# Performance work log

Hardware: AMD Instinct MI355X
Metric: run time of the kernel (lower is better)

## Reference

```python
import jax, jax.numpy as jnp
import numpy as np

B, L = 256, 100
N100, N10_100, N0_10 = 40000, 80000, 120000
D100, D10_100, D0_10 = 500, 250, 250  # layers[0]/2, layers[0]/4, remainder
H1, H2 = 200, 1000                    # layers = [1000, 200, 1000]
NUM_PIX = N100 + N10_100 + N0_10


def setup_inputs() -> dict:
    key = jax.random.key(0)
    ks = jax.random.split(key, 11)
    rn = lambda k, shape, scale: jax.random.normal(k, shape, jnp.float32) * scale
    return {
        'songs_bucket': jax.random.randint(ks[0], (B, L), 0, 3, jnp.int32),
        'songs_id': jax.random.randint(ks[1], (B, L), 0, N100, jnp.int32),
        'W100': rn(ks[2], (N100, D100), 0.02),
        'W10_100': rn(ks[3], (N10_100, D10_100), 0.02),
        'W0_10': rn(ks[4], (N0_10, D0_10), 0.02),
        'fc1_w': rn(ks[5], (H1, 1000), 0.03),
        'fc1_b': jnp.zeros((H1,), jnp.float32),
        'fc2_w': rn(ks[6], (H2, H1), 0.07),
        'fc2_b': jnp.zeros((H2,), jnp.float32),
        'out_w': rn(ks[7], (NUM_PIX, H2), 0.03),
        'out_b': jnp.zeros((NUM_PIX,), jnp.float32),
    }


def _masked_mean(table, ids, mask):
    # table: [V, D], ids: [B, L], mask: [B, L] bool -> [B, D]
    emb = table[ids]                                   # gather [B, L, D]
    m = mask.astype(emb.dtype)
    ssum = jnp.einsum('bl,bld->bd', m, emb)            # masked segment-sum
    cnt = m.sum(axis=1)                                # [B]
    mean = ssum / jnp.maximum(cnt, 1.0)[:, None]
    return jnp.where(cnt[:, None] > 0, mean, 0.0)     # empty bucket -> zeros


def reference(songs_bucket, songs_id, W100, W10_100, W0_10,
              fc1_w, fc1_b, fc2_w, fc2_b, out_w, out_b):
    # per-bucket masked embedding mean (vectorized embedding-bag)
    e0 = _masked_mean(W100, songs_id, songs_bucket == 0)       # [B, 500]
    e1 = _masked_mean(W10_100, songs_id, songs_bucket == 1)    # [B, 250]
    e2 = _masked_mean(W0_10, songs_id, songs_bucket == 2)      # [B, 250]
    x = jnp.concatenate([e0, e1, e2], axis=-1)                 # [B, 1000]
    # tiny MLP (dropout p=False -> p=0, a no-op)
    h = jax.nn.relu(x @ fc1_w.T + fc1_b)                       # [B, 200]
    h = jax.nn.relu(h @ fc2_w.T + fc2_b)                       # [B, 1000]
    ratings = h @ out_w.T + out_b                              # [B, NUM_PIX]
    return ratings
```

## Files before the change

kernel.cpp:

```cpp
#include <hip/hip_runtime.h>

#define NUM_B 256
#define SEQ_L 100
#define NPIX  240000
#define KPAD  1024
#define BN    128
#define BK    128
#define NWG   1875

typedef __attribute__((ext_vector_type(8))) short short8;
typedef __attribute__((ext_vector_type(4))) float f32x4;

static __device__ __forceinline__ unsigned short f2bf(float f) {
  unsigned int u = __builtin_bit_cast(unsigned int, f);
  u += 0x7fffu + ((u >> 16) & 1u);
  return (unsigned short)(u >> 16);
}

__global__ __launch_bounds__(1024) void embed_mlp_kernel(
    const int* __restrict__ bucket, const int* __restrict__ ids,
    const float* __restrict__ W100, const float* __restrict__ W10,
    const float* __restrict__ W0,
    const float* __restrict__ fc1_w, const float* __restrict__ fc1_b,
    const float* __restrict__ fc2_w, const float* __restrict__ fc2_b,
    unsigned short* __restrict__ h2out)
{
  __shared__ __align__(16) float xw[16][1000];
  __shared__ __align__(16) float xs[1000];
  __shared__ __align__(16) float h1s[200];
  __shared__ int sb[SEQ_L], sid[SEQ_L];
  __shared__ int cnt[16][3];
  __shared__ int cntT[3];

  const int row = blockIdx.x, tid = threadIdx.x;
  const int wid = tid >> 6, lane = tid & 63;

  if (tid < SEQ_L) {
    sb[tid]  = bucket[row * SEQ_L + tid];
    sid[tid] = ids[row * SEQ_L + tid];
  }
  __syncthreads();

  float acc0[8] = {0,0,0,0,0,0,0,0};
  float acc1[4] = {0,0,0,0};
  float acc2[4] = {0,0,0,0};
  int c0 = 0, c1 = 0, c2 = 0;

  for (int l = wid; l < SEQ_L; l += 16) {
    const int b = sb[l];
    const long id = sid[l];
    if (b == 0) {
      ++c0; const float* r = W100 + id * 500;
      #pragma unroll
      for (int j = 0; j < 7; ++j) acc0[j] += r[lane + 64 * j];
      if (lane < 52) acc0[7] += r[lane + 448];
    } else if (b == 1) {
      ++c1; const float* r = W10 + id * 250;
      #pragma unroll
      for (int j = 0; j < 3; ++j) acc1[j] += r[lane + 64 * j];
      if (lane < 58) acc1[3] += r[lane + 192];
    } else {
      ++c2; const float* r = W0 + id * 250;
      #pragma unroll
      for (int j = 0; j < 3; ++j) acc2[j] += r[lane + 64 * j];
      if (lane < 58) acc2[3] += r[lane + 192];
    }
  }
  {
    float* xp = xw[wid];
    #pragma unroll
    for (int j = 0; j < 8; ++j) { int d = lane + 64 * j; if (d < 500) xp[d] = acc0[j]; }
    #pragma unroll
    for (int j = 0; j < 4; ++j) { int d = lane + 64 * j; if (d < 250) xp[500 + d] = acc1[j]; }
    #pragma unroll
    for (int j = 0; j < 4; ++j) { int d = lane + 64 * j; if (d < 250) xp[750 + d] = acc2[j]; }
    if (lane == 0) { cnt[wid][0] = c0; cnt[wid][1] = c1; cnt[wid][2] = c2; }
  }
  __syncthreads();
  if (tid < 3) { int s = 0; for (int w = 0; w < 16; ++w) s += cnt[w][tid]; cntT[tid] = s; }
  __syncthreads();
  if (tid < 1000) {
    float s = 0.f;
    #pragma unroll
    for (int w = 0; w < 16; ++w) s += xw[w][tid];
    const int bkt = tid < 500 ? 0 : (tid < 750 ? 1 : 2);
    const int c = cntT[bkt];
    xs[tid] = c ? s / (float)c : 0.f;
  }
  __syncthreads();

  const int g = tid >> 4, sl = tid & 15;

  for (int o = g; o < 200; o += 64) {
    const f32x4* wr = (const f32x4*)(fc1_w + o * 1000);
    const f32x4* xv = (const f32x4*)xs;
    float p = 0.f;
    for (int j = sl; j < 250; j += 16) {
      f32x4 a = xv[j], b = wr[j];
      p += a.x * b.x + a.y * b.y + a.z * b.z + a.w * b.w;
    }
    #pragma unroll
    for (int off = 8; off; off >>= 1) p += __shfl_down(p, off, 16);
    if (sl == 0) h1s[o] = fmaxf(p + fc1_b[o], 0.f);
  }
  __syncthreads();

  unsigned short* hrow = h2out + (long)row * KPAD;
  for (int o = g; o < 1000; o += 64) {
    const f32x4* wr = (const f32x4*)(fc2_w + o * 200);
    const f32x4* hv = (const f32x4*)h1s;
    float p = 0.f;
    #pragma unroll
    for (int j = sl; j < 50; j += 16) {
      f32x4 a = hv[j], b = wr[j];
      p += a.x * b.x + a.y * b.y + a.z * b.z + a.w * b.w;
    }
    #pragma unroll
    for (int off = 8; off; off >>= 1) p += __shfl_down(p, off, 16);
    if (sl == 0) hrow[o] = f2bf(fmaxf(p + fc2_b[o], 0.f));
  }
  if (tid < KPAD - 1000) hrow[1000 + tid] = 0;
}

__global__ __launch_bounds__(512) void out_gemm_kernel(
    const unsigned short* __restrict__ h2,
    const float* __restrict__ out_w,
    const float* __restrict__ out_b,
    float* __restrict__ out)
{
  __shared__ __align__(16) unsigned char lds[98304];
  unsigned char* As = lds;
  unsigned char* Bs = lds + 65536;

  const int tid = threadIdx.x;

  const int q = NWG / 8, r = NWG % 8;
  const int xcd = blockIdx.x & 7, bidx = blockIdx.x >> 3;
  const int wg = (xcd < r ? xcd * (q + 1) : r * (q + 1) + (xcd - r) * q) + bidx;
  const long n0 = (long)wg * BN;

  const f32x4 fz = {0.f, 0.f, 0.f, 0.f};

  f32x4 bReg[8];

  auto dmaA = [&](int kt) {
    #pragma unroll
    for (int i = 0; i < 8; ++i) {
      const int c = tid + 512 * i;
      const int rw = c >> 4;
      const int k16s = (c & 15) ^ (rw & 7);
      const unsigned short* src = h2 + rw * KPAD + kt * BK + k16s * 8;
      __builtin_amdgcn_global_load_lds(
          (const __attribute__((address_space(1))) void*)src,
          (__attribute__((address_space(3))) void*)(As + c * 16),
          16, 0, 0);
    }
  };
  auto loadB = [&](int k0) {
    #pragma unroll
    for (int i = 0; i < 8; ++i) {
      int c = tid + 512 * i;
      int n = c >> 5, qq = c & 31;
      int k = k0 + qq * 4;
      bReg[i] = (k < 1000)
        ? __builtin_nontemporal_load((const f32x4*)(out_w + (long)(n0 + n) * 1000 + k))
        : fz;
    }
  };
  auto storeB = [&]() {
    #pragma unroll
    for (int i = 0; i < 8; ++i) {
      int c = tid + 512 * i;
      int n = c >> 5, qq = c & 31;
      ushort4 h;
      h.x = f2bf(bReg[i].x); h.y = f2bf(bReg[i].y);
      h.z = f2bf(bReg[i].z); h.w = f2bf(bReg[i].w);
      *(ushort4*)(Bs + n * 256 + ((qq * 8) ^ ((n & 7) << 4))) = h;
    }
  };

  const int wid = tid >> 6, lane = tid & 63;
  const int wm = wid >> 2, wn = wid & 3;
  const int lrow = lane & 15, lkg = lane >> 4;

  f32x4 acc[8][2];
  #pragma unroll
  for (int m = 0; m < 8; ++m) { acc[m][0] = fz; acc[m][1] = fz; }

  dmaA(0); loadB(0);
  #pragma unroll 1
  for (int kt = 0; kt < 8; ++kt) {
    storeB();
    __syncthreads();
    if (kt < 7) loadB((kt + 1) * BK);
    #pragma unroll
    for (int kk = 0; kk < 4; ++kk) {
      short8 bf[2];
      #pragma unroll
      for (int n = 0; n < 2; ++n) {
        int nr = wn * 32 + n * 16 + lrow;
        bf[n] = *(const short8*)(Bs + nr * 256 + (((kk * 64) + lkg * 16) ^ ((nr & 7) << 4)));
      }
      #pragma unroll
      for (int m = 0; m < 8; ++m) {
        int rr = wm * 128 + m * 16 + lrow;
        short8 af = *(const short8*)(As + rr * 256 + (((kk * 64) + lkg * 16) ^ ((rr & 7) << 4)));
        acc[m][0] = __builtin_amdgcn_mfma_f32_16x16x32_bf16(af, bf[0], acc[m][0], 0, 0, 0);
        acc[m][1] = __builtin_amdgcn_mfma_f32_16x16x32_bf16(af, bf[1], acc[m][1], 0, 0, 0);
      }
    }
    __syncthreads();
    if (kt < 7) dmaA((kt + 1) * 0 + kt + 1);
  }

  const float b0 = out_b[n0 + wn * 32 + lrow];
  const float b1 = out_b[n0 + wn * 32 + 16 + lrow];
  float* E = (float*)lds;
  #pragma unroll
  for (int half = 0; half < 2; ++half) {
    __syncthreads();
    if (wm == half) {
      #pragma unroll
      for (int m = 0; m < 8; ++m) {
        #pragma unroll
        for (int n = 0; n < 2; ++n) {
          const int col = wn * 32 + n * 16 + lrow;
          const float bias = n ? b1 : b0;
          #pragma unroll
          for (int rr = 0; rr < 4; ++rr) {
            const int rowl = m * 16 + lkg * 4 + rr;
            E[rowl * 132 + col] = acc[m][n][rr] + bias;
          }
        }
      }
    }
    __syncthreads();
    const int rbase = half * 128;
    #pragma unroll
    for (int s = 0; s < 8; ++s) {
      const int rowl = s * 16 + (tid >> 5);
      const int c = (tid & 31) * 4;
      f32x4 v = *(const f32x4*)(E + rowl * 132 + c);
      __builtin_nontemporal_store(v, (f32x4*)(out + (long)(rbase + rowl) * NPIX + n0 + c));
    }
  }
}

extern "C" void kernel_launch(void* const* d_in, const int* in_sizes, int n_in,
                              void* d_out, int out_size, void* d_ws, size_t ws_size,
                              hipStream_t stream) {
  const int*   bucket = (const int*)d_in[0];
  const int*   ids    = (const int*)d_in[1];
  const float* W100   = (const float*)d_in[2];
  const float* W10    = (const float*)d_in[3];
  const float* W0     = (const float*)d_in[4];
  const float* fc1w   = (const float*)d_in[5];
  const float* fc1b   = (const float*)d_in[6];
  const float* fc2w   = (const float*)d_in[7];
  const float* fc2b   = (const float*)d_in[8];
  const float* outw   = (const float*)d_in[9];
  const float* outb   = (const float*)d_in[10];
  float* out = (float*)d_out;
  unsigned short* h2w = (unsigned short*)d_ws;

  embed_mlp_kernel<<<NUM_B, 1024, 0, stream>>>(bucket, ids, W100, W10, W0,
                                               fc1w, fc1b, fc2w, fc2b, h2w);
  out_gemm_kernel<<<NWG, 512, 0, stream>>>(h2w, outw, outb, out);
}
```

Measured before the change: 319.7 us.

## Double-buffer B tile in LDS with explicit waitcnt-based software pipeline

Restructures the out_gemm main loop into a two-stage pipeline. B goes into two LDS buffers with two register sets, and explicit s_waitcnt vmcnt/lgkmcnt barriers plus sched_barriers let the next global loads stay in flight while the MFMAs run on the current tile. The aim is to hide the out_w streaming latency that the old load/store/sync loop exposed. It raises LDS use to 128KB and register pressure, which could lower occupancy. Correctness depends on the hand-set vmcnt counts matching the number of outstanding loads.

```diff
diff --git a/kernel.cpp b/kernel.cpp
--- a/kernel.cpp
+++ b/kernel.cpp
@@ -128,9 +128,10 @@
     const float* __restrict__ out_b,
     float* __restrict__ out)
 {
-  __shared__ __align__(16) unsigned char lds[98304];
-  unsigned char* As = lds;
-  unsigned char* Bs = lds + 65536;
+  __shared__ __align__(16) unsigned char lds[131072];
+  unsigned char* As  = lds;
+  unsigned char* Bs0 = lds + 65536;
+  unsigned char* Bs1 = lds + 98304;
 
   const int tid = threadIdx.x;
 
@@ -141,7 +142,7 @@
 
   const f32x4 fz = {0.f, 0.f, 0.f, 0.f};
 
-  f32x4 bReg[8];
+  f32x4 bE[8], bO[8];
 
   auto dmaA = [&](int kt) {
     #pragma unroll
@@ -156,25 +157,25 @@
           16, 0, 0);
     }
   };
-  auto loadB = [&](int k0) {
+  auto loadB = [&](f32x4* bR, int kt) {
     #pragma unroll
     for (int i = 0; i < 8; ++i) {
       int c = tid + 512 * i;
       int n = c >> 5, qq = c & 31;
-      int k = k0 + qq * 4;
-      bReg[i] = (k < 1000)
+      int k = kt * BK + qq * 4;
+      bR[i] = (k < 1000)
         ? __builtin_nontemporal_load((const f32x4*)(out_w + (long)(n0 + n) * 1000 + k))
         : fz;
     }
   };
-  auto storeB = [&]() {
+  auto storeB = [&](const f32x4* bR, unsigned char* Bs) {
     #pragma unroll
     for (int i = 0; i < 8; ++i) {
       int c = tid + 512 * i;
       int n = c >> 5, qq = c & 31;
       ushort4 h;
-      h.x = f2bf(bReg[i].x); h.y = f2bf(bReg[i].y);
-      h.z = f2bf(bReg[i].z); h.w = f2bf(bReg[i].w);
+      h.x = f2bf(bR[i].x); h.y = f2bf(bR[i].y);
+      h.z = f2bf(bR[i].z); h.w = f2bf(bR[i].w);
       *(ushort4*)(Bs + n * 256 + ((qq * 8) ^ ((n & 7) << 4))) = h;
     }
   };
@@ -187,12 +188,7 @@
   #pragma unroll
   for (int m = 0; m < 8; ++m) { acc[m][0] = fz; acc[m][1] = fz; }
 
-  dmaA(0); loadB(0);
-  #pragma unroll 1
-  for (int kt = 0; kt < 8; ++kt) {
-    storeB();
-    __syncthreads();
-    if (kt < 7) loadB((kt + 1) * BK);
+  auto compute = [&](const unsigned char* Bs) {
     #pragma unroll
     for (int kk = 0; kk < 4; ++kk) {
       short8 bf[2];
@@ -209,9 +205,50 @@
         acc[m][1] = __builtin_amdgcn_mfma_f32_16x16x32_bf16(af, bf[1], acc[m][1], 0, 0, 0);
       }
     }
-    __syncthreads();
-    if (kt < 7) dmaA((kt + 1) * 0 + kt + 1);
-  }
+  };
+
+  #define SCHED()   __builtin_amdgcn_sched_barrier(0)
+  #define LGKMBAR() do { asm volatile("s_waitcnt lgkmcnt(0)" ::: "memory"); \
+                         __builtin_amdgcn_s_barrier(); SCHED(); } while (0)
+  #define VM8BAR()  do { asm volatile("s_waitcnt vmcnt(8) lgkmcnt(0)" ::: "memory"); \
+                         __builtin_amdgcn_s_barrier(); SCHED(); } while (0)
+  #define VM0BAR()  do { asm volatile("s_waitcnt vmcnt(0) lgkmcnt(0)" ::: "memory"); \
+                         __builtin_amdgcn_s_barrier(); SCHED(); } while (0)
+
+  loadB(bE, 0);
+  dmaA(0); SCHED();
+  storeB(bE, Bs0);
+  loadB(bO, 1);
+  VM8BAR();
+
+  #pragma unroll 1
+  for (int i = 0; i < 3; ++i) {
+    compute(Bs0);
+    LGKMBAR();
+    dmaA(2 * i + 1); SCHED();
+    storeB(bO, Bs1);
+    loadB(bE, 2 * i + 2);
+    VM8BAR();
+
+    compute(Bs1);
+    LGKMBAR();
+    dmaA(2 * i + 2); SCHED();
+    storeB(bE, Bs0);
+    loadB(bO, 2 * i + 3);
+    VM8BAR();
+  }
+
+  compute(Bs0);
+  LGKMBAR();
+  dmaA(7); SCHED();
+  storeB(bO, Bs1);
+  VM0BAR();
+  compute(Bs1);
+
+  #undef SCHED
+  #undef LGKMBAR
+  #undef VM8BAR
+  #undef VM0BAR
 
   const float b0 = out_b[n0 + wn * 32 + lrow];
   const float b1 = out_b[n0 + wn * 32 + 16 + lrow];
```

Result: slower. 330.9 us (+3.5%).
